# Optimization experiments

Measured on AMD Instinct MI355X. Metric: run time of the kernel, lower is better.

The kernel has to match this reference:

```python
import jax, jax.numpy as jnp
import numpy as np

EPS = 1e-8  # args.epsilon
B, N, D = 2, 512, 64


def _cmul(ar, ai, br, bi):
    # complex Hadamard: (ar+i ai)(br+i bi)
    return ar * br - ai * bi, ar * bi + ai * br


def _clin(Z, W, b):
    # complex linear: Z [B,2,N,din], W [2,dout,din], b [2,dout]
    yr = Z[:, 0] @ W[0].T - Z[:, 1] @ W[1].T + b[0]
    yi = Z[:, 0] @ W[1].T + Z[:, 1] @ W[0].T + b[1]
    return yr, yi


def setup_inputs() -> dict:
    key = jax.random.key(0)
    ks = jax.random.split(key, 12)
    s = 1.0 / np.sqrt(D)
    inp = {
        "Z_q": jax.random.normal(ks[0], (B, 2, N, D), jnp.float32),
        "Z_k": jax.random.normal(ks[1], (B, 2, N, D), jnp.float32),
        "Z_v": jax.random.normal(ks[2], (B, 2, N, D), jnp.float32),
        "t_measure_all": (jnp.arange(N + 1, dtype=jnp.float32) / N)[None, :],
        "Wq_w": jax.random.normal(ks[3], (2, D, D), jnp.float32) * s,
        "Wq_b": jax.random.normal(ks[4], (2, D), jnp.float32) * 0.02,
        "Wk_w": jax.random.normal(ks[5], (2, D, D), jnp.float32) * s,
        "Wk_b": jax.random.normal(ks[6], (2, D), jnp.float32) * 0.02,
        "Wv_w": jax.random.normal(ks[7], (2, D, D), jnp.float32) * s,
        "Wv_b": jax.random.normal(ks[8], (2, D), jnp.float32) * 0.02,
        "Wp_w": jax.random.normal(ks[9], (2, D, D), jnp.float32) * s,
        "Wp_b": jax.random.normal(ks[10], (2, D), jnp.float32) * 0.02,
        "lambda_imag_v": jax.random.normal(ks[11], (D // 2,), jnp.float32),
        "lambda_omega_sqrt_v": jnp.asarray(0.5, jnp.float32),
        "lambda_gamma_sqrt_v": jnp.asarray(0.5, jnp.float32),
        "noise_floor": jnp.asarray(1.0, jnp.float32),
        "tau": jnp.asarray(1.0, jnp.float32),
        "eta_param": jnp.zeros((D,), jnp.float32),
    }
    return inp


def reference(Z_q, Z_k, Z_v, t_measure_all, Wq_w, Wq_b, Wk_w, Wk_b, Wv_w, Wv_b,
              Wp_w, Wp_b, lambda_imag_v, lambda_omega_sqrt_v, lambda_gamma_sqrt_v,
              noise_floor, tau, eta_param):
    n = Z_q.shape[2]
    # eigenvalues: lambda_real_zero==1 -> real part 0; conjugate imaginary pairs
    lam_imag = jnp.concatenate([lambda_imag_v, -lambda_imag_v])  # (D,)
    lambda_h = jnp.stack([jnp.zeros_like(lam_imag), lam_imag])   # (2, D)

    t = t_measure_all[0, :-1]
    t = t / (t[-1] - t[0])

    # exp kernels exp(+/- lambda t); real part 0 => pure phase
    ph = t[:, None] * lam_imag[None, :]            # (N, D)
    ef_r, ef_i = jnp.cos(ph), jnp.sin(ph)          # exp(+lambda t) (= V_v = V_k, mat_exp)
    eb_r, eb_i = ef_r, -ef_i                       # exp(-lambda t)

    Qr, Qi = _clin(Z_q, Wq_w, Wq_b)                # (B, N, D)
    Kr, Ki = _clin(Z_k, Wk_w, Wk_b)
    Vr, Vi = _clin(Z_v, Wv_w, Wv_b)

    # backward-propagated factors U = exp(-lambda t) o {Q,K,V}
    Uq_r, Uq_i = _cmul(eb_r, eb_i, Qr, Qi)
    Uk_r, Uk_i = _cmul(eb_r, eb_i, Kr, Ki)
    Uv_r, Uv_i = _cmul(eb_r, eb_i, Vr, Vi)

    # scalar covariance kernel (zero real part -> linear-in-|dt| variance)
    lambda_omega = lambda_omega_sqrt_v ** 2
    lambda_gamma = lambda_gamma_sqrt_v ** 2 + EPS
    V_avg = lambda_omega * jnp.abs(t[:, None] - t[None, :]) + lambda_gamma  # (N, N)

    # weighted residual norm R_ij = sum_d |V_k_i o (U_q_i - U_k_j)|^2, expanded
    W2 = ef_r ** 2 + ef_i ** 2                     # (N, D)  |V_k|^2
    aq2 = Uq_r ** 2 + Uq_i ** 2
    ak2 = Uk_r ** 2 + Uk_i ** 2
    t1 = jnp.einsum('id,bid->bi', W2, aq2)[:, :, None]
    t2 = jnp.einsum('id,bjd->bij', W2, ak2)
    t3 = (jnp.einsum('bid,bjd->bij', W2[None] * Uq_r, Uk_r)
          + jnp.einsum('bid,bjd->bij', W2[None] * Uq_i, Uk_i))
    R = t1 + t2 - 2.0 * t3                         # (B, N, N)

    base = (noise_floor ** 2 + EPS) * V_avg[None] + R
    scores = -(tau ** 2) * jnp.log(base)
    mask = jnp.tril(jnp.ones((n, n), bool))
    scores = jnp.where(mask[None], scores, -jnp.inf)
    A = jax.nn.softmax(scores, axis=2)             # (B, N, N)

    # est_inner = Q_ij @ U_v (Q_ij imag part is zero)
    er = jnp.einsum('bij,bjd->bid', A, Uv_r)
    ei = jnp.einsum('bij,bjd->bid', A, Uv_i)
    estv_r, estv_i = _cmul(ef_r, ef_i, er, ei)     # V_v o est_inner

    eta = jax.nn.sigmoid(eta_param)                # (D,)
    g = jax.nn.sigmoid(eta)                        # faithful double sigmoid
    elr = (1.0 - eta) * Vr + g * estv_r
    eli = (1.0 - eta) * Vi + g * estv_i

    pr, pi = _cmul(ef_r, ef_i, elr, eli)           # mat_exp o est_latent
    P = jnp.stack([pr, pi], axis=1)
    or_, oi_ = _clin(P, Wp_w, Wp_b)
    out = jnp.stack([or_, oi_], axis=1)            # (B, 2, N, D)

    est_latent = jnp.stack([elr, eli], axis=1)
    Q_ij = jnp.stack([A, jnp.zeros_like(A)], axis=1)
    # Z_ij_hat_all[b,:,i,j,d] = V_v_i o U_v_j  (propagated estimates)
    Zr = ef_r[None, :, None, :] * Uv_r[:, None] - ef_i[None, :, None, :] * Uv_i[:, None]
    Zi = ef_r[None, :, None, :] * Uv_i[:, None] + ef_i[None, :, None, :] * Uv_r[:, None]
    Z_ij_hat_all = jnp.stack([Zr, Zi], axis=1)     # (B, 2, N, N, D)

    return est_latent, out, Q_ij, Z_ij_hat_all, lambda_h
```

## Files before the change

### kernel.cpp

```cpp
#include <hip/hip_runtime.h>
#include <math.h>

#define NB 512
#define ND 64
#define EPSF 1e-8f

__global__ __launch_bounds__(64) void proj_kernel(
    const float* __restrict__ Zq, const float* __restrict__ Zk, const float* __restrict__ Zv,
    const float* __restrict__ tma,
    const float* __restrict__ Wq_w, const float* __restrict__ Wq_b,
    const float* __restrict__ Wk_w, const float* __restrict__ Wk_b,
    const float* __restrict__ Wv_w, const float* __restrict__ Wv_b,
    const float* __restrict__ lam_v,
    float* __restrict__ ef_r, float* __restrict__ ef_i,
    float* __restrict__ Uq_r, float* __restrict__ Uq_i,
    float* __restrict__ Uk_r, float* __restrict__ Uk_i,
    float* __restrict__ Uv_r, float* __restrict__ Uv_i,
    float* __restrict__ Vr_o, float* __restrict__ Vi_o,
    float* __restrict__ sumq, float* __restrict__ sumk,
    float* __restrict__ lam_out)
{
    const int bn = blockIdx.x;
    const int b  = bn >> 9;
    const int n  = bn & (NB - 1);
    const int d  = threadIdx.x;

    __shared__ float zqr[ND], zqi[ND], zkr[ND], zki[ND], zvr[ND], zvi[ND];
    zqr[d] = Zq[((b*2 + 0)*NB + n)*ND + d];
    zqi[d] = Zq[((b*2 + 1)*NB + n)*ND + d];
    zkr[d] = Zk[((b*2 + 0)*NB + n)*ND + d];
    zki[d] = Zk[((b*2 + 1)*NB + n)*ND + d];
    zvr[d] = Zv[((b*2 + 0)*NB + n)*ND + d];
    zvi[d] = Zv[((b*2 + 1)*NB + n)*ND + d];
    __syncthreads();

    const float lam = (d < 32) ? lam_v[d] : -lam_v[d - 32];
    const float t0    = tma[0];
    const float denom = tma[NB - 1] - t0;
    const float tn    = tma[n] / denom;
    const float ph  = tn * lam;
    const float efr = cosf(ph);
    const float efi = sinf(ph);

    if (b == 0) { ef_r[n*ND + d] = efr; ef_i[n*ND + d] = efi; }
    if (bn == 0) { lam_out[d] = 0.0f; lam_out[ND + d] = lam; }

    float qr = Wq_b[d], qi = Wq_b[ND + d];
    float kr = Wk_b[d], ki = Wk_b[ND + d];
    float vr = Wv_b[d], vi = Wv_b[ND + d];
    const int r0 = d * ND;
    const int r1 = ND*ND + d * ND;
    #pragma unroll 8
    for (int e = 0; e < ND; ++e) {
        const float w0q = Wq_w[r0 + e], w1q = Wq_w[r1 + e];
        qr += zqr[e]*w0q - zqi[e]*w1q;
        qi += zqr[e]*w1q + zqi[e]*w0q;
        const float w0k = Wk_w[r0 + e], w1k = Wk_w[r1 + e];
        kr += zkr[e]*w0k - zki[e]*w1k;
        ki += zkr[e]*w1k + zki[e]*w0k;
        const float w0v = Wv_w[r0 + e], w1v = Wv_w[r1 + e];
        vr += zvr[e]*w0v - zvi[e]*w1v;
        vi += zvr[e]*w1v + zvi[e]*w0v;
    }

    const float uqr = efr*qr + efi*qi, uqi = efr*qi - efi*qr;
    const float ukr = efr*kr + efi*ki, uki = efr*ki - efi*kr;
    const float uvr = efr*vr + efi*vi, uvi = efr*vi - efi*vr;

    const int idx = bn*ND + d;
    Uq_r[idx] = uqr; Uq_i[idx] = uqi;
    Uk_r[idx] = ukr; Uk_i[idx] = uki;
    Uv_r[idx] = uvr; Uv_i[idx] = uvi;
    Vr_o[idx] = vr;  Vi_o[idx] = vi;

    float q2 = uqr*uqr + uqi*uqi;
    float k2 = ukr*ukr + uki*uki;
    #pragma unroll
    for (int off = 32; off > 0; off >>= 1) {
        q2 += __shfl_down(q2, off);
        k2 += __shfl_down(k2, off);
    }
    if (d == 0) { sumq[bn] = q2; sumk[bn] = k2; }
}

__global__ __launch_bounds__(256) void attn_kernel(
    const float* __restrict__ ef_r, const float* __restrict__ ef_i,
    const float* __restrict__ Uq_r, const float* __restrict__ Uq_i,
    const float* __restrict__ Uk_r, const float* __restrict__ Uk_i,
    const float* __restrict__ Uv_r, const float* __restrict__ Uv_i,
    const float* __restrict__ Vr,  const float* __restrict__ Vi,
    const float* __restrict__ sumq, const float* __restrict__ sumk,
    const float* __restrict__ tma,
    const float* __restrict__ eta_param,
    const float* __restrict__ s_lo, const float* __restrict__ s_lg,
    const float* __restrict__ s_nf, const float* __restrict__ s_tau,
    float* __restrict__ estl_out,
    float* __restrict__ Q_out,
    float* __restrict__ p_r, float* __restrict__ p_i)
{
    const int bi  = blockIdx.x;
    const int b   = bi >> 9;
    const int i   = bi & (NB - 1);
    const int tid = threadIdx.x;

    __shared__ __align__(16) float sA[NB];
    __shared__ __align__(16) float qr_s[ND], qi_s[ND];
    __shared__ float red[256];
    __shared__ float erp[8][ND];

    const float t0    = tma[0];
    const float denom = tma[NB - 1] - t0;
    const float ti    = tma[i] / denom;
    const float lo    = s_lo[0] * s_lo[0];
    const float lg    = s_lg[0] * s_lg[0] + EPSF;
    const float nf2   = s_nf[0] * s_nf[0] + EPSF;
    const float tau2  = s_tau[0] * s_tau[0];
    const float t1    = sumq[bi];

    if (tid < ND) { qr_s[tid] = Uq_r[bi*ND + tid]; qi_s[tid] = Uq_i[bi*ND + tid]; }
    __syncthreads();

    float lmax = -INFINITY;
    for (int j = tid; j <= i; j += 256) {
        const float4* kr4 = (const float4*)&Uk_r[(b*NB + j)*ND];
        const float4* ki4 = (const float4*)&Uk_i[(b*NB + j)*ND];
        const float4* qr4 = (const float4*)qr_s;
        const float4* qi4 = (const float4*)qi_s;
        float dot = 0.0f;
        #pragma unroll
        for (int e = 0; e < ND/4; ++e) {
            const float4 kr = kr4[e], ki = ki4[e];
            const float4 qr = qr4[e], qi = qi4[e];
            dot += qr.x*kr.x + qr.y*kr.y + qr.z*kr.z + qr.w*kr.w
                 + qi.x*ki.x + qi.y*ki.y + qi.z*ki.z + qi.w*ki.w;
        }
        const float tj   = tma[j] / denom;
        const float vavg = lo * fabsf(ti - tj) + lg;
        const float base = nf2 * vavg + t1 + sumk[b*NB + j] - 2.0f*dot;
        const float sc   = -tau2 * logf(base);
        sA[j] = sc;
        lmax = fmaxf(lmax, sc);
    }

    red[tid] = lmax; __syncthreads();
    for (int s = 128; s > 0; s >>= 1) {
        if (tid < s) red[tid] = fmaxf(red[tid], red[tid + s]);
        __syncthreads();
    }
    const float m = red[0];
    __syncthreads();

    float lsum = 0.0f;
    for (int j = tid; j <= i; j += 256) {
        const float e = expf(sA[j] - m);
        sA[j] = e;
        lsum += e;
    }
    red[tid] = lsum; __syncthreads();
    for (int s = 128; s > 0; s >>= 1) {
        if (tid < s) red[tid] += red[tid + s];
        __syncthreads();
    }
    const float inv = 1.0f / red[0];
    __syncthreads();

    for (int j = tid; j < NB; j += 256) {
        float a = 0.0f;
        if (j <= i) { a = sA[j] * inv; sA[j] = a; }
        Q_out[((size_t)(b*2 + 0)*NB + i)*NB + j] = a;
        Q_out[((size_t)(b*2 + 1)*NB + i)*NB + j] = 0.0f;
    }
    __syncthreads();

    const int lane = tid & 63;
    const int w    = tid >> 6;
    float er = 0.0f, ei = 0.0f;
    for (int j = w; j <= i; j += 4) {
        const float a = sA[j];
        er += a * Uv_r[(b*NB + j)*ND + lane];
        ei += a * Uv_i[(b*NB + j)*ND + lane];
    }
    erp[w][lane] = er; erp[4 + w][lane] = ei;
    __syncthreads();

    if (tid < ND) {
        const int d = tid;
        const float err = erp[0][d] + erp[1][d] + erp[2][d] + erp[3][d];
        const float eii = erp[4][d] + erp[5][d] + erp[6][d] + erp[7][d];
        const float efr = ef_r[i*ND + d], efi = ef_i[i*ND + d];
        const float estr = efr*err - efi*eii;
        const float esti = efr*eii + efi*err;
        const float eta  = 1.0f / (1.0f + expf(-eta_param[d]));
        const float g    = 1.0f / (1.0f + expf(-eta));
        const float vr   = Vr[bi*ND + d], vi = Vi[bi*ND + d];
        const float elr  = (1.0f - eta)*vr + g*estr;
        const float eli  = (1.0f - eta)*vi + g*esti;
        estl_out[((b*2 + 0)*NB + i)*ND + d] = elr;
        estl_out[((b*2 + 1)*NB + i)*ND + d] = eli;
        p_r[bi*ND + d] = efr*elr - efi*eli;
        p_i[bi*ND + d] = efr*eli + efi*elr;
    }
}

__global__ __launch_bounds__(64) void outproj_kernel(
    const float* __restrict__ p_r, const float* __restrict__ p_i,
    const float* __restrict__ Wp_w, const float* __restrict__ Wp_b,
    float* __restrict__ out)
{
    const int bn = blockIdx.x;
    const int b  = bn >> 9;
    const int n  = bn & (NB - 1);
    const int d  = threadIdx.x;

    __shared__ float pr[ND], pi[ND];
    pr[d] = p_r[bn*ND + d];
    pi[d] = p_i[bn*ND + d];
    __syncthreads();

    float orr = Wp_b[d], oii = Wp_b[ND + d];
    const int r0 = d * ND;
    const int r1 = ND*ND + d * ND;
    #pragma unroll 8
    for (int e = 0; e < ND; ++e) {
        const float w0 = Wp_w[r0 + e], w1 = Wp_w[r1 + e];
        orr += pr[e]*w0 - pi[e]*w1;
        oii += pr[e]*w1 + pi[e]*w0;
    }
    out[((b*2 + 0)*NB + n)*ND + d] = orr;
    out[((b*2 + 1)*NB + n)*ND + d] = oii;
}

__global__ __launch_bounds__(256) void zhat_kernel(
    const float* __restrict__ ef_r, const float* __restrict__ ef_i,
    const float* __restrict__ Uv_r, const float* __restrict__ Uv_i,
    float* __restrict__ Z_out)
{
    const int bi  = blockIdx.x;
    const int b   = bi >> 9;
    const int i   = bi & (NB - 1);
    const int tid = threadIdx.x;

    __shared__ __align__(16) float efr_s[ND], efi_s[ND];
    if (tid < ND) { efr_s[tid] = ef_r[i*ND + tid]; efi_s[tid] = ef_i[i*ND + tid]; }
    __syncthreads();

    const int d0    = (tid * 4) & (ND - 1);
    const int jbase = (tid * 4) >> 6;
    const float4 er4 = *(const float4*)&efr_s[d0];
    const float4 ei4 = *(const float4*)&efi_s[d0];

    const size_t base_r = ((size_t)(b*2 + 0)*NB + i) * (size_t)(NB*ND);
    const size_t base_i = ((size_t)(b*2 + 1)*NB + i) * (size_t)(NB*ND);

    for (int jg = 0; jg < NB; jg += 16) {
        const int j = jg + jbase;
        const float4 uvr = *(const float4*)&Uv_r[(b*NB + j)*ND + d0];
        const float4 uvi = *(const float4*)&Uv_i[(b*NB + j)*ND + d0];
        float4 zr, zi;
        zr.x = er4.x*uvr.x - ei4.x*uvi.x;  zi.x = er4.x*uvi.x + ei4.x*uvr.x;
        zr.y = er4.y*uvr.y - ei4.y*uvi.y;  zi.y = er4.y*uvi.y + ei4.y*uvr.y;
        zr.z = er4.z*uvr.z - ei4.z*uvi.z;  zi.z = er4.z*uvi.z + ei4.z*uvr.z;
        zr.w = er4.w*uvr.w - ei4.w*uvi.w;  zi.w = er4.w*uvi.w + ei4.w*uvr.w;
        const size_t off = (size_t)j*ND + d0;
        *(float4*)&Z_out[base_r + off] = zr;
        *(float4*)&Z_out[base_i + off] = zi;
    }
}

extern "C" void kernel_launch(void* const* d_in, const int* in_sizes, int n_in,
                              void* d_out, int out_size, void* d_ws, size_t ws_size,
                              hipStream_t stream) {
    const float* Zq   = (const float*)d_in[0];
    const float* Zk   = (const float*)d_in[1];
    const float* Zv   = (const float*)d_in[2];
    const float* tma  = (const float*)d_in[3];
    const float* Wq_w = (const float*)d_in[4];
    const float* Wq_b = (const float*)d_in[5];
    const float* Wk_w = (const float*)d_in[6];
    const float* Wk_b = (const float*)d_in[7];
    const float* Wv_w = (const float*)d_in[8];
    const float* Wv_b = (const float*)d_in[9];
    const float* Wp_w = (const float*)d_in[10];
    const float* Wp_b = (const float*)d_in[11];
    const float* lamv = (const float*)d_in[12];
    const float* s_lo = (const float*)d_in[13];
    const float* s_lg = (const float*)d_in[14];
    const float* s_nf = (const float*)d_in[15];
    const float* s_tau= (const float*)d_in[16];
    const float* etap = (const float*)d_in[17];

    float* out = (float*)d_out;
    float* o_est = out;
    float* o_out = out + 131072;
    float* o_Q   = out + 262144;
    float* o_Z   = out + 1310720;
    float* o_lam = out + 68419584;

    float* ws   = (float*)d_ws;
    float* ef_r = ws;
    float* ef_i = ws + 32768;
    float* Uq_r = ws + 65536;
    float* Uq_i = ws + 131072;
    float* Uk_r = ws + 196608;
    float* Uk_i = ws + 262144;
    float* Uv_r = ws + 327680;
    float* Uv_i = ws + 393216;
    float* Vr   = ws + 458752;
    float* Vi   = ws + 524288;
    float* p_r  = ws + 589824;
    float* p_i  = ws + 655360;
    float* sumq = ws + 720896;
    float* sumk = ws + 721920;

    proj_kernel<<<2*NB, 64, 0, stream>>>(Zq, Zk, Zv, tma, Wq_w, Wq_b, Wk_w, Wk_b,
        Wv_w, Wv_b, lamv, ef_r, ef_i, Uq_r, Uq_i, Uk_r, Uk_i, Uv_r, Uv_i,
        Vr, Vi, sumq, sumk, o_lam);

    attn_kernel<<<2*NB, 256, 0, stream>>>(ef_r, ef_i, Uq_r, Uq_i, Uk_r, Uk_i,
        Uv_r, Uv_i, Vr, Vi, sumq, sumk, tma, etap, s_lo, s_lg, s_nf, s_tau,
        o_est, o_Q, p_r, p_i);

    outproj_kernel<<<2*NB, 64, 0, stream>>>(p_r, p_i, Wp_w, Wp_b, o_out);

    zhat_kernel<<<2*NB, 256, 0, stream>>>(ef_r, ef_i, Uv_r, Uv_i, o_Z);
}
```

Measured before the change: 398.9 us.

## Fuse attention, output projection and Z-hat write into one kernel

Merges the attention, output-projection and Z_ij_hat kernels into a single per-row kernel. The Z-hat stream writes are issued at the start of each block, and the output projection runs from shared memory split across four waves. This removes two launches and the p_r/p_i round trip through global memory. In exchange each block now carries the large Z store traffic in front of the attention work, which could change occupancy and the latency profile.

```diff
diff --git a/kernel.cpp b/kernel.cpp
--- a/kernel.cpp
+++ b/kernel.cpp
@@ -83,7 +83,7 @@
     if (d == 0) { sumq[bn] = q2; sumk[bn] = k2; }
 }
 
-__global__ __launch_bounds__(256) void attn_kernel(
+__global__ __launch_bounds__(256) void mega_kernel(
     const float* __restrict__ ef_r, const float* __restrict__ ef_i,
     const float* __restrict__ Uq_r, const float* __restrict__ Uq_i,
     const float* __restrict__ Uk_r, const float* __restrict__ Uk_i,
@@ -94,19 +94,53 @@
     const float* __restrict__ eta_param,
     const float* __restrict__ s_lo, const float* __restrict__ s_lg,
     const float* __restrict__ s_nf, const float* __restrict__ s_tau,
+    const float* __restrict__ Wp_w, const float* __restrict__ Wp_b,
     float* __restrict__ estl_out,
+    float* __restrict__ out_o,
     float* __restrict__ Q_out,
-    float* __restrict__ p_r, float* __restrict__ p_i)
+    float* __restrict__ Z_out)
 {
     const int bi  = blockIdx.x;
     const int b   = bi >> 9;
     const int i   = bi & (NB - 1);
     const int tid = threadIdx.x;
 
+    __shared__ __align__(16) float efr_s[ND], efi_s[ND];
     __shared__ __align__(16) float sA[NB];
     __shared__ __align__(16) float qr_s[ND], qi_s[ND];
     __shared__ float red[256];
     __shared__ float erp[8][ND];
+    __shared__ float pr_s[ND], pi_s[ND];
+
+    if (tid < ND) {
+        efr_s[tid] = ef_r[i*ND + tid];
+        efi_s[tid] = ef_i[i*ND + tid];
+        qr_s[tid]  = Uq_r[bi*ND + tid];
+        qi_s[tid]  = Uq_i[bi*ND + tid];
+    }
+    __syncthreads();
+
+    {
+        const int d0    = (tid * 4) & (ND - 1);
+        const int jbase = tid >> 4;
+        const float4 er4 = *(const float4*)&efr_s[d0];
+        const float4 ei4 = *(const float4*)&efi_s[d0];
+        const size_t base_r = ((size_t)(b*2 + 0)*NB + i) * (size_t)(NB*ND);
+        const size_t base_i = ((size_t)(b*2 + 1)*NB + i) * (size_t)(NB*ND);
+        for (int jg = 0; jg < NB; jg += 16) {
+            const int j = jg + jbase;
+            const float4 uvr = *(const float4*)&Uv_r[(b*NB + j)*ND + d0];
+            const float4 uvi = *(const float4*)&Uv_i[(b*NB + j)*ND + d0];
+            float4 zr, zi;
+            zr.x = er4.x*uvr.x - ei4.x*uvi.x;  zi.x = er4.x*uvi.x + ei4.x*uvr.x;
+            zr.y = er4.y*uvr.y - ei4.y*uvi.y;  zi.y = er4.y*uvi.y + ei4.y*uvr.y;
+            zr.z = er4.z*uvr.z - ei4.z*uvi.z;  zi.z = er4.z*uvi.z + ei4.z*uvr.z;
+            zr.w = er4.w*uvr.w - ei4.w*uvi.w;  zi.w = er4.w*uvi.w + ei4.w*uvr.w;
+            const size_t off = (size_t)j*ND + d0;
+            *(float4*)&Z_out[base_r + off] = zr;
+            *(float4*)&Z_out[base_i + off] = zi;
+        }
+    }
 
     const float t0    = tma[0];
     const float denom = tma[NB - 1] - t0;
@@ -116,9 +150,6 @@
     const float nf2   = s_nf[0] * s_nf[0] + EPSF;
     const float tau2  = s_tau[0] * s_tau[0];
     const float t1    = sumq[bi];
-
-    if (tid < ND) { qr_s[tid] = Uq_r[bi*ND + tid]; qi_s[tid] = Uq_i[bi*ND + tid]; }
-    __syncthreads();
 
     float lmax = -INFINITY;
     for (int j = tid; j <= i; j += 256) {
@@ -174,20 +205,23 @@
 
     const int lane = tid & 63;
     const int w    = tid >> 6;
-    float er = 0.0f, ei = 0.0f;
-    for (int j = w; j <= i; j += 4) {
-        const float a = sA[j];
-        er += a * Uv_r[(b*NB + j)*ND + lane];
-        ei += a * Uv_i[(b*NB + j)*ND + lane];
-    }
-    erp[w][lane] = er; erp[4 + w][lane] = ei;
+    {
+        float er = 0.0f, ei = 0.0f;
+        #pragma unroll 4
+        for (int j = w; j <= i; j += 4) {
+            const float a = sA[j];
+            er += a * Uv_r[(b*NB + j)*ND + lane];
+            ei += a * Uv_i[(b*NB + j)*ND + lane];
+        }
+        erp[w][lane] = er; erp[4 + w][lane] = ei;
+    }
     __syncthreads();
 
     if (tid < ND) {
         const int d = tid;
         const float err = erp[0][d] + erp[1][d] + erp[2][d] + erp[3][d];
         const float eii = erp[4][d] + erp[5][d] + erp[6][d] + erp[7][d];
-        const float efr = ef_r[i*ND + d], efi = ef_i[i*ND + d];
+        const float efr = efr_s[d], efi = efi_s[d];
         const float estr = efr*err - efi*eii;
         const float esti = efr*eii + efi*err;
         const float eta  = 1.0f / (1.0f + expf(-eta_param[d]));
@@ -197,73 +231,33 @@
         const float eli  = (1.0f - eta)*vi + g*esti;
         estl_out[((b*2 + 0)*NB + i)*ND + d] = elr;
         estl_out[((b*2 + 1)*NB + i)*ND + d] = eli;
-        p_r[bi*ND + d] = efr*elr - efi*eli;
-        p_i[bi*ND + d] = efr*eli + efi*elr;
-    }
-}
-
-__global__ __launch_bounds__(64) void outproj_kernel(
-    const float* __restrict__ p_r, const float* __restrict__ p_i,
-    const float* __restrict__ Wp_w, const float* __restrict__ Wp_b,
-    float* __restrict__ out)
-{
-    const int bn = blockIdx.x;
-    const int b  = bn >> 9;
-    const int n  = bn & (NB - 1);
-    const int d  = threadIdx.x;
-
-    __shared__ float pr[ND], pi[ND];
-    pr[d] = p_r[bn*ND + d];
-    pi[d] = p_i[bn*ND + d];
-    __syncthreads();
-
-    float orr = Wp_b[d], oii = Wp_b[ND + d];
-    const int r0 = d * ND;
-    const int r1 = ND*ND + d * ND;
-    #pragma unroll 8
-    for (int e = 0; e < ND; ++e) {
-        const float w0 = Wp_w[r0 + e], w1 = Wp_w[r1 + e];
-        orr += pr[e]*w0 - pi[e]*w1;
-        oii += pr[e]*w1 + pi[e]*w0;
-    }
-    out[((b*2 + 0)*NB + n)*ND + d] = orr;
-    out[((b*2 + 1)*NB + n)*ND + d] = oii;
-}
-
-__global__ __launch_bounds__(256) void zhat_kernel(
-    const float* __restrict__ ef_r, const float* __restrict__ ef_i,
-    const float* __restrict__ Uv_r, const float* __restrict__ Uv_i,
-    float* __restrict__ Z_out)
-{
-    const int bi  = blockIdx.x;
-    const int b   = bi >> 9;
-    const int i   = bi & (NB - 1);
-    const int tid = threadIdx.x;
-
-    __shared__ __align__(16) float efr_s[ND], efi_s[ND];
-    if (tid < ND) { efr_s[tid] = ef_r[i*ND + tid]; efi_s[tid] = ef_i[i*ND + tid]; }
-    __syncthreads();
-
-    const int d0    = (tid * 4) & (ND - 1);
-    const int jbase = (tid * 4) >> 6;
-    const float4 er4 = *(const float4*)&efr_s[d0];
-    const float4 ei4 = *(const float4*)&efi_s[d0];
-
-    const size_t base_r = ((size_t)(b*2 + 0)*NB + i) * (size_t)(NB*ND);
-    const size_t base_i = ((size_t)(b*2 + 1)*NB + i) * (size_t)(NB*ND);
-
-    for (int jg = 0; jg < NB; jg += 16) {
-        const int j = jg + jbase;
-        const float4 uvr = *(const float4*)&Uv_r[(b*NB + j)*ND + d0];
-        const float4 uvi = *(const float4*)&Uv_i[(b*NB + j)*ND + d0];
-        float4 zr, zi;
-        zr.x = er4.x*uvr.x - ei4.x*uvi.x;  zi.x = er4.x*uvi.x + ei4.x*uvr.x;
-        zr.y = er4.y*uvr.y - ei4.y*uvi.y;  zi.y = er4.y*uvi.y + ei4.y*uvr.y;
-        zr.z = er4.z*uvr.z - ei4.z*uvi.z;  zi.z = er4.z*uvi.z + ei4.z*uvr.z;
-        zr.w = er4.w*uvr.w - ei4.w*uvi.w;  zi.w = er4.w*uvi.w + ei4.w*uvr.w;
-        const size_t off = (size_t)j*ND + d0;
-        *(float4*)&Z_out[base_r + off] = zr;
-        *(float4*)&Z_out[base_i + off] = zi;
+        pr_s[d] = efr*elr - efi*eli;
+        pi_s[d] = efr*eli + efi*elr;
+    }
+    __syncthreads();
+
+    {
+        const int d = lane;
+        const int q = w;
+        float orr = 0.0f, oii = 0.0f;
+        const int r0 = d * ND;
+        const int r1 = ND*ND + d * ND;
+        #pragma unroll
+        for (int e = q*16; e < q*16 + 16; ++e) {
+            const float w0 = Wp_w[r0 + e], w1 = Wp_w[r1 + e];
+            orr += pr_s[e]*w0 - pi_s[e]*w1;
+            oii += pr_s[e]*w1 + pi_s[e]*w0;
+        }
+        erp[q][d] = orr; erp[4 + q][d] = oii;
+    }
+    __syncthreads();
+
+    if (tid < ND) {
+        const int d = tid;
+        const float orr = erp[0][d] + erp[1][d] + erp[2][d] + erp[3][d] + Wp_b[d];
+        const float oii = erp[4][d] + erp[5][d] + erp[6][d] + erp[7][d] + Wp_b[ND + d];
+        out_o[((b*2 + 0)*NB + i)*ND + d] = orr;
+        out_o[((b*2 + 1)*NB + i)*ND + d] = oii;
     }
 }
 
@@ -307,20 +301,14 @@
     float* Uv_i = ws + 393216;
     float* Vr   = ws + 458752;
     float* Vi   = ws + 524288;
-    float* p_r  = ws + 589824;
-    float* p_i  = ws + 655360;
-    float* sumq = ws + 720896;
-    float* sumk = ws + 721920;
+    float* sumq = ws + 589824;
+    float* sumk = ws + 590848;
 
     proj_kernel<<<2*NB, 64, 0, stream>>>(Zq, Zk, Zv, tma, Wq_w, Wq_b, Wk_w, Wk_b,
         Wv_w, Wv_b, lamv, ef_r, ef_i, Uq_r, Uq_i, Uk_r, Uk_i, Uv_r, Uv_i,
         Vr, Vi, sumq, sumk, o_lam);
 
-    attn_kernel<<<2*NB, 256, 0, stream>>>(ef_r, ef_i, Uq_r, Uq_i, Uk_r, Uk_i,
+    mega_kernel<<<2*NB, 256, 0, stream>>>(ef_r, ef_i, Uq_r, Uq_i, Uk_r, Uk_i,
         Uv_r, Uv_i, Vr, Vi, sumq, sumk, tma, etap, s_lo, s_lg, s_nf, s_tau,
-        o_est, o_Q, p_r, p_i);
-
-    outproj_kernel<<<2*NB, 64, 0, stream>>>(p_r, p_i, Wp_w, Wp_b, o_out);
-
-    zhat_kernel<<<2*NB, 256, 0, stream>>>(ef_r, ef_i, Uv_r, Uv_i, o_Z);
+        Wp_w, Wp_b, o_est, o_out, o_Q, o_Z);
 }
```

Result: no change. 405.9 us (+1.8%).
